# Kernel tuning notes

Hardware: AMD Instinct MI355X
Metric: run time of the kernel (lower is better)

## Reference

```python
import jax, jax.numpy as jnp
import numpy as np
import math

B, S, D, OUT, H = 512, 80, 768, 768, 12


def setup_inputs() -> dict:
    key = jax.random.key(0)
    ks = jax.random.split(key, 8)
    scale = 0.02
    hidden = jax.random.normal(ks[0], (B, S, D), dtype=jnp.float32)
    mask = jnp.ones((B, S), dtype=jnp.int32)
    Wq = jax.random.normal(ks[1], (D, D), dtype=jnp.float32) * scale
    bq = jax.random.normal(ks[2], (D,), dtype=jnp.float32) * scale
    Wk = jax.random.normal(ks[3], (D, D), dtype=jnp.float32) * scale
    bk = jax.random.normal(ks[4], (D,), dtype=jnp.float32) * scale
    Wv = jax.random.normal(ks[5], (D, OUT), dtype=jnp.float32) * scale
    bv = jax.random.normal(ks[6], (OUT,), dtype=jnp.float32) * scale
    return {"hidden": hidden, "mask": mask, "Wq": Wq, "bq": bq,
            "Wk": Wk, "bk": bk, "Wv": Wv, "bv": bv}


def _rope_tables(seq_len, head_dim, dtype):
    # RoE_QAndK(seq_len): standard RoPE, emb = cat([sin, cos], -1), chunked
    half = head_dim // 2
    inv_freq = 1.0 / (10000.0 ** (np.arange(0, half, dtype=np.float32) * 2.0 / head_dim))
    pos = np.arange(seq_len, dtype=np.float32)
    freqs = pos[:, None] * inv_freq[None, :]  # [S, half]
    return jnp.asarray(np.sin(freqs), dtype), jnp.asarray(np.cos(freqs), dtype)


def _rotate(x, sin, cos):
    # interleaved RoPE: even/odd channels
    x1, x2 = x[..., 0::2], x[..., 1::2]
    out = jnp.stack([x1 * cos - x2 * sin, x2 * cos + x1 * sin], axis=-1)
    return out.reshape(x.shape)


def reference(hidden, mask, Wq, bq, Wk, bk, Wv, bv):
    b, s, d = hidden.shape
    dh = Wq.shape[1] // H   # query/key head dim
    dv = Wv.shape[1] // H   # value head dim

    def split_heads(x, hd):
        return x.reshape(b, s, H, hd).transpose(0, 2, 1, 3)  # [b,h,s,hd]

    q = split_heads(hidden @ Wq + bq, dh)
    k = split_heads(hidden @ Wk + bk, dh)
    v = split_heads(hidden @ Wv + bv, dv)

    sin, cos = _rope_tables(s, dh, hidden.dtype)  # [s, dh//2]
    q = _rotate(q, sin, cos)
    k = _rotate(k, sin, cos)

    bias = (1.0 - mask.astype(hidden.dtype))[:, None, None, :] * -10000.0
    scores = jnp.einsum('bhqd,bhkd->bhqk', q, k) / math.sqrt(dh) + bias
    prob = jax.nn.softmax(scores, axis=-1)  # dropout is identity in eval
    ctx = jnp.einsum('bhqk,bhkd->bhqd', prob, v)
    return ctx.transpose(0, 2, 1, 3).reshape(b, s, H * dv)
```

## Files before the change

kernel.cpp:

```cpp
#include <hip/hip_runtime.h>
#include <hip/hip_bf16.h>
#include <stdint.h>

#define H_    12
#define B_    512
#define S_    80
#define D_    768
#define NQKV  2304
#define DH    64

typedef __bf16 bf16x8 __attribute__((ext_vector_type(8)));
typedef float  f32x4  __attribute__((ext_vector_type(4)));
typedef unsigned short u16;
typedef unsigned int   u32;

__device__ __forceinline__ u16 f2bf(float f) {
    u32 u = __builtin_bit_cast(u32, f);
    u32 r = u + 0x7FFFu + ((u >> 16) & 1u);
    return (u16)(r >> 16);
}
__device__ __forceinline__ float bf2f(u16 h) {
    u32 u = ((u32)h) << 16;
    return __builtin_bit_cast(float, u);
}

__device__ __forceinline__ void gload16(const void* g, void* l) {
    __builtin_amdgcn_global_load_lds((const __attribute__((address_space(1))) void*)g,
                                     (__attribute__((address_space(3))) void*)l, 16, 0, 0);
}

#define VMCNT(n) asm volatile("s_waitcnt vmcnt(" #n ")" ::: "memory")
#define BARRIER() do { asm volatile("" ::: "memory"); __builtin_amdgcn_s_barrier(); asm volatile("" ::: "memory"); } while (0)

#define TRB 432
#define CVB 1616

__global__ __launch_bounds__(256) void prep_fused(
    const float* __restrict__ X,
    const float* __restrict__ Wq, const float* __restrict__ bq,
    const float* __restrict__ Wk, const float* __restrict__ bk,
    const float* __restrict__ Wv, const float* __restrict__ bv,
    u16* __restrict__ Wt, float* __restrict__ biasf,
    float* __restrict__ ropeS, float* __restrict__ ropeC,
    u16* __restrict__ Xb)
{
    const int tid = threadIdx.x;
    if (blockIdx.x < TRB) {
        __shared__ u16 T[64][72];
        int t = blockIdx.x;
        int mat = t / 144;
        int rem = t - mat * 144;
        int kb = (rem / 12) * 64;
        int nb = (rem % 12) * 64;
        const float* W = (mat == 0) ? Wq : (mat == 1 ? Wk : Wv);
        int r  = tid >> 2;
        int q4 = tid & 3;
#pragma unroll
        for (int i = 0; i < 4; ++i) {
            float4 v = *reinterpret_cast<const float4*>(&W[(size_t)(kb + r) * D_ + nb + q4 * 16 + i * 4]);
            T[q4 * 16 + i * 4 + 0][r] = f2bf(v.x);
            T[q4 * 16 + i * 4 + 1][r] = f2bf(v.y);
            T[q4 * 16 + i * 4 + 2][r] = f2bf(v.z);
            T[q4 * 16 + i * 4 + 3][r] = f2bf(v.w);
        }
        __syncthreads();
        int n_local = tid >> 2;
        int kq = tid & 3;
        uint4 o0 = *reinterpret_cast<const uint4*>(&T[n_local][kq * 16]);
        uint4 o1 = *reinterpret_cast<const uint4*>(&T[n_local][kq * 16 + 8]);
        u16* dst = &Wt[(size_t)(mat * D_ + nb + n_local) * D_ + kb + kq * 16];
        *reinterpret_cast<uint4*>(dst) = o0;
        *reinterpret_cast<uint4*>(dst + 8) = o1;
    } else {
        int gidx = (blockIdx.x - TRB) * 256 + tid;
        const int gstride = CVB * 256;
        for (int i = gidx; i < NQKV; i += gstride) {
            const float* bsrc; int nn;
            if (i < D_)          { bsrc = bq; nn = i; }
            else if (i < 2 * D_) { bsrc = bk; nn = i - D_; }
            else                 { bsrc = bv; nn = i - 2 * D_; }
            biasf[i] = bsrc[nn];
        }
        for (int i = gidx; i < S_ * 32; i += gstride) {
            int pos = i >> 5, fi = i & 31;
            float invf = powf(10000.0f, -(float)fi / 32.0f);
            float fr = (float)pos * invf;
            ropeS[i] = sinf(fr);
            ropeC[i] = cosf(fr);
        }
        const int n4 = 40960 * D_ / 4;
        for (int i = gidx; i < n4; i += gstride) {
            float4 v = reinterpret_cast<const float4*>(X)[i];
            uint2 u;
            u.x = (u32)f2bf(v.x) | ((u32)f2bf(v.y) << 16);
            u.y = (u32)f2bf(v.z) | ((u32)f2bf(v.w) << 16);
            reinterpret_cast<uint2*>(Xb)[i] = u;
        }
    }
}

#define BK 64
#define NT 12
#define CLD 264

__global__ __launch_bounds__(512, 2) void qkv_gemm(
    const u16*   __restrict__ Xb,
    const u16*   __restrict__ Wt,
    const float* __restrict__ biasf,
    u16*         __restrict__ Y)
{
    __shared__ alignas(16) u16 smem[65536];

    const int orig = blockIdx.x;
    const int swz = (orig & 7) * 180 + (orig >> 3);
    const int m0 = (swz / 9) * 256;
    const int n0 = (swz % 9) * 256;

    const int tid = threadIdx.x;
    const int lane = tid & 63;
    const int w  = tid >> 6;
    const int wr = w >> 2;
    const int wc = w & 3;
    const int lr = lane & 15;
    const int lg = lane >> 4;

    const int srow = tid >> 3;
    const int scol = ((tid & 7) ^ (srow & 7)) << 3;

    f32x4 acc[8][4] = {};
    bf16x8 af[2][4], bf[2][4];

#define STAGE_A(p, h, q, kt) \
    gload16(&Xb[(size_t)(m0 + (h)*128 + (q)*64 + srow) * D_ + (kt)*BK + scol], \
            &smem[(p)*32768 + (h)*8192 + (q)*4096 + w*512])
#define STAGE_B(p, hb, jj, kt) \
    gload16(&Wt[(size_t)(n0 + (hb)*128 + (jj)*64 + srow) * D_ + (kt)*BK + scol], \
            &smem[(p)*32768 + 16384 + (hb)*8192 + (jj)*4096 + w*512])
#define LDA_F(p, rr, kk_) \
    (*reinterpret_cast<const bf16x8*>(&smem[(p)*32768 + wr*8192 + (rr)*64 + ((((kk_)*4 + lg) ^ ((rr) & 7)) << 3)]))
#define LDB_F(p, rb, kk_) \
    (*reinterpret_cast<const bf16x8*>(&smem[(p)*32768 + 16384 + (wc>>1)*8192 + (rb)*64 + ((((kk_)*4 + lg) ^ ((rb) & 7)) << 3)]))

    STAGE_A(0, 0, 0, 0); STAGE_A(0, 1, 0, 0);
    STAGE_B(0, 0, 0, 0); STAGE_B(0, 0, 1, 0);
    STAGE_B(0, 1, 0, 0); STAGE_B(0, 1, 1, 0);
    STAGE_A(0, 0, 1, 0); STAGE_A(0, 1, 1, 0);
    VMCNT(2);
    BARRIER();

#pragma unroll
    for (int u = 0; u < NT - 1; ++u) {
        const int p = u & 1, pn = p ^ 1, kt1 = u + 1;
#pragma unroll
        for (int kk = 0; kk < 2; ++kk) {
#pragma unroll
            for (int ii = 0; ii < 4; ++ii) af[kk][ii] = LDA_F(p, ii * 16 + lr, kk);
#pragma unroll
            for (int jj = 0; jj < 2; ++jj) bf[kk][jj] = LDB_F(p, (wc & 1) * 64 + jj * 16 + lr, kk);
        }
        STAGE_A(pn, 0, 0, kt1); STAGE_A(pn, 1, 0, kt1);
        STAGE_B(pn, 0, 0, kt1); STAGE_B(pn, 0, 1, kt1);
        BARRIER();
        __builtin_amdgcn_s_setprio(1);
#pragma unroll
        for (int kk = 0; kk < 2; ++kk)
#pragma unroll
            for (int ii = 0; ii < 4; ++ii)
#pragma unroll
                for (int jj = 0; jj < 2; ++jj)
                    acc[ii][jj] = __builtin_amdgcn_mfma_f32_16x16x32_bf16(af[kk][ii], bf[kk][jj], acc[ii][jj], 0, 0, 0);
        __builtin_amdgcn_s_setprio(0);
#pragma unroll
        for (int kk = 0; kk < 2; ++kk)
#pragma unroll
            for (int jj = 2; jj < 4; ++jj) bf[kk][jj] = LDB_F(p, (wc & 1) * 64 + jj * 16 + lr, kk);
        STAGE_B(pn, 1, 0, kt1); STAGE_B(pn, 1, 1, kt1);
        VMCNT(6);
        BARRIER();
        __builtin_amdgcn_s_setprio(1);
#pragma unroll
        for (int kk = 0; kk < 2; ++kk)
#pragma unroll
            for (int ii = 0; ii < 4; ++ii)
#pragma unroll
                for (int jj = 0; jj < 2; ++jj)
                    acc[ii][jj + 2] = __builtin_amdgcn_mfma_f32_16x16x32_bf16(af[kk][ii], bf[kk][jj + 2], acc[ii][jj + 2], 0, 0, 0);
        __builtin_amdgcn_s_setprio(0);
#pragma unroll
        for (int kk = 0; kk < 2; ++kk)
#pragma unroll
            for (int ii = 0; ii < 4; ++ii) af[kk][ii] = LDA_F(p, 64 + ii * 16 + lr, kk);
        STAGE_A(pn, 0, 1, kt1); STAGE_A(pn, 1, 1, kt1);
        BARRIER();
        __builtin_amdgcn_s_setprio(1);
#pragma unroll
        for (int kk = 0; kk < 2; ++kk)
#pragma unroll
            for (int ii = 0; ii < 4; ++ii)
#pragma unroll
                for (int jj = 0; jj < 2; ++jj)
                    acc[ii + 4][jj] = __builtin_amdgcn_mfma_f32_16x16x32_bf16(af[kk][ii], bf[kk][jj], acc[ii + 4][jj], 0, 0, 0);
        __builtin_amdgcn_s_setprio(0);
        VMCNT(2);
        BARRIER();
        __builtin_amdgcn_s_setprio(1);
#pragma unroll
        for (int kk = 0; kk < 2; ++kk)
#pragma unroll
            for (int ii = 0; ii < 4; ++ii)
#pragma unroll
                for (int jj = 0; jj < 2; ++jj)
                    acc[ii + 4][jj + 2] = __builtin_amdgcn_mfma_f32_16x16x32_bf16(af[kk][ii], bf[kk][jj + 2], acc[ii + 4][jj + 2], 0, 0, 0);
        __builtin_amdgcn_s_setprio(0);
    }
    {
        const int p = 1;
#pragma unroll
        for (int kk = 0; kk < 2; ++kk) {
#pragma unroll
            for (int ii = 0; ii < 4; ++ii) af[kk][ii] = LDA_F(p, ii * 16 + lr, kk);
#pragma unroll
            for (int jj = 0; jj < 2; ++jj) bf[kk][jj] = LDB_F(p, (wc & 1) * 64 + jj * 16 + lr, kk);
        }
        BARRIER();
#pragma unroll
        for (int kk = 0; kk < 2; ++kk)
#pragma unroll
            for (int ii = 0; ii < 4; ++ii)
#pragma unroll
                for (int jj = 0; jj < 2; ++jj)
                    acc[ii][jj] = __builtin_amdgcn_mfma_f32_16x16x32_bf16(af[kk][ii], bf[kk][jj], acc[ii][jj], 0, 0, 0);
#pragma unroll
        for (int kk = 0; kk < 2; ++kk)
#pragma unroll
            for (int jj = 2; jj < 4; ++jj) bf[kk][jj] = LDB_F(p, (wc & 1) * 64 + jj * 16 + lr, kk);
        VMCNT(0);
        BARRIER();
#pragma unroll
        for (int kk = 0; kk < 2; ++kk)
#pragma unroll
            for (int ii = 0; ii < 4; ++ii)
#pragma unroll
                for (int jj = 0; jj < 2; ++jj)
                    acc[ii][jj + 2] = __builtin_amdgcn_mfma_f32_16x16x32_bf16(af[kk][ii], bf[kk][jj + 2], acc[ii][jj + 2], 0, 0, 0);
#pragma unroll
        for (int kk = 0; kk < 2; ++kk)
#pragma unroll
            for (int ii = 0; ii < 4; ++ii) af[kk][ii] = LDA_F(p, 64 + ii * 16 + lr, kk);
        BARRIER();
#pragma unroll
        for (int kk = 0; kk < 2; ++kk)
#pragma unroll
            for (int ii = 0; ii < 4; ++ii)
#pragma unroll
                for (int jj = 0; jj < 2; ++jj)
                    acc[ii + 4][jj] = __builtin_amdgcn_mfma_f32_16x16x32_bf16(af[kk][ii], bf[kk][jj], acc[ii + 4][jj], 0, 0, 0);
        BARRIER();
#pragma unroll
        for (int kk = 0; kk < 2; ++kk)
#pragma unroll
            for (int ii = 0; ii < 4; ++ii)
#pragma unroll
                for (int jj = 0; jj < 2; ++jj)
                    acc[ii + 4][jj + 2] = __builtin_amdgcn_mfma_f32_16x16x32_bf16(af[kk][ii], bf[kk][jj + 2], acc[ii + 4][jj + 2], 0, 0, 0);
    }

    float bias_v[4];
#pragma unroll
    for (int j = 0; j < 4; ++j) bias_v[j] = biasf[n0 + wc * 64 + j * 16 + lr];

    __syncthreads();
#pragma unroll
    for (int hh = 0; hh < 2; ++hh) {
        if (wr == hh) {
#pragma unroll
            for (int i = 0; i < 8; ++i)
#pragma unroll
                for (int j = 0; j < 4; ++j)
#pragma unroll
                    for (int r = 0; r < 4; ++r)
                        smem[(i * 16 + lg * 4 + r) * CLD + wc * 64 + j * 16 + lr] = f2bf(acc[i][j][r] + bias_v[j]);
        }
        __syncthreads();
#pragma unroll
        for (int pp = 0; pp < 8; ++pp) {
            int idx = pp * 512 + tid;
            int row = idx >> 5, ch = idx & 31;
            uint4 v = *reinterpret_cast<const uint4*>(&smem[row * CLD + ch * 8]);
            *reinterpret_cast<uint4*>(&Y[(size_t)(m0 + hh * 128 + row) * NQKV + n0 + ch * 8]) = v;
        }
        __syncthreads();
    }
#undef STAGE_A
#undef STAGE_B
#undef LDA_F
#undef LDB_F
}

#define LQ 72
#define LV 104

__device__ __forceinline__ u32 rope_rot(u32 u, float sn, float cs, float scale) {
    float x1 = bf2f((u16)(u & 0xffff)), x2 = bf2f((u16)(u >> 16));
    float o1 = (x1 * cs - x2 * sn) * scale;
    float o2 = (x2 * cs + x1 * sn) * scale;
    return (u32)f2bf(o1) | ((u32)f2bf(o2) << 16);
}

__global__ __launch_bounds__(320) void attn_kernel(
    const u16* __restrict__ Y,
    const int* __restrict__ mask,
    const float* __restrict__ ropeS,
    const float* __restrict__ ropeC,
    float* __restrict__ out)
{
    __shared__ alignas(16) u16 Qs[S_ * LQ];
    __shared__ alignas(16) u16 Ks[S_ * LQ];
    __shared__ alignas(16) u16 Vt[DH * LV];
    __shared__ alignas(16) u16 Ps[5 * 16 * LV];
    __shared__ float biasS[S_];

    const int h = blockIdx.x;
    const int b = blockIdx.y;
    const int tid = threadIdx.x;
    const size_t rowbase = (size_t)b * S_ * NQKV;

#pragma unroll
    for (int it = 0; it < 4; ++it) {
        int ch = it * 320 + tid;
        int q = ch >> 4;
        int sub = ch & 15;
        int isK = sub >> 3;
        int c0 = (sub & 7) * 8;
        uint4 v = *reinterpret_cast<const uint4*>(&Y[rowbase + (size_t)q * NQKV + isK * D_ + h * DH + c0]);
        float4 sn4 = *reinterpret_cast<const float4*>(&ropeS[q * 32 + c0 / 2]);
        float4 cs4 = *reinterpret_cast<const float4*>(&ropeC[q * 32 + c0 / 2]);
        float scale = isK ? 1.0f : 0.125f;
        uint4 o;
        o.x = rope_rot(v.x, sn4.x, cs4.x, scale);
        o.y = rope_rot(v.y, sn4.y, cs4.y, scale);
        o.z = rope_rot(v.z, sn4.z, cs4.z, scale);
        o.w = rope_rot(v.w, sn4.w, cs4.w, scale);
        u16* dst = isK ? Ks : Qs;
        *reinterpret_cast<uint4*>(&dst[q * LQ + c0]) = o;
    }
#pragma unroll
    for (int it = 0; it < 2; ++it) {
        int ch = it * 320 + tid;
        int s = ch >> 3, c0 = (ch & 7) * 8;
        uint4 v = *reinterpret_cast<const uint4*>(&Y[rowbase + (size_t)s * NQKV + 2 * D_ + h * DH + c0]);
        Vt[(c0 + 0) * LV + s] = (u16)(v.x & 0xffff);
        Vt[(c0 + 1) * LV + s] = (u16)(v.x >> 16);
        Vt[(c0 + 2) * LV + s] = (u16)(v.y & 0xffff);
        Vt[(c0 + 3) * LV + s] = (u16)(v.y >> 16);
        Vt[(c0 + 4) * LV + s] = (u16)(v.z & 0xffff);
        Vt[(c0 + 5) * LV + s] = (u16)(v.z >> 16);
        Vt[(c0 + 6) * LV + s] = (u16)(v.w & 0xffff);
        Vt[(c0 + 7) * LV + s] = (u16)(v.w >> 16);
    }
    for (int e = tid; e < DH * 16; e += 320) {
        int c = e >> 4, s = 80 + (e & 15);
        Vt[c * LV + s] = 0;
    }
    for (int e = tid; e < S_ * 16; e += 320) {
        int row = e >> 4, col = 80 + (e & 15);
        Ps[row * LV + col] = 0;
    }
    for (int e = tid; e < S_; e += 320)
        biasS[e] = (1.0f - (float)mask[b * S_ + e]) * -10000.0f;
    __syncthreads();

    const int wv = tid >> 6;
    const int lane = tid & 63;
    const int lr = lane & 15;
    const int lg = lane >> 4;

    f32x4 sc[5] = {};
    bf16x8 aq[2];
#pragma unroll
    for (int kk = 0; kk < 2; ++kk)
        aq[kk] = *reinterpret_cast<const bf16x8*>(&Qs[(wv * 16 + lr) * LQ + kk * 32 + lg * 8]);
#pragma unroll
    for (int t = 0; t < 5; ++t) {
#pragma unroll
        for (int kk = 0; kk < 2; ++kk) {
            bf16x8 bk8 = *reinterpret_cast<const bf16x8*>(&Ks[(t * 16 + lr) * LQ + kk * 32 + lg * 8]);
            sc[t] = __builtin_amdgcn_mfma_f32_16x16x32_bf16(aq[kk], bk8, sc[t], 0, 0, 0);
        }
    }
#pragma unroll
    for (int j = 0; j < 4; ++j) {
        float m = -1e30f;
#pragma unroll
        for (int t = 0; t < 5; ++t) { sc[t][j] += biasS[t * 16 + lr]; m = fmaxf(m, sc[t][j]); }
#pragma unroll
        for (int msk = 1; msk < 16; msk <<= 1) m = fmaxf(m, __shfl_xor(m, msk));
        float s = 0.f;
#pragma unroll
        for (int t = 0; t < 5; ++t) { float e = __expf(sc[t][j] - m); sc[t][j] = e; s += e; }
#pragma unroll
        for (int msk = 1; msk < 16; msk <<= 1) s += __shfl_xor(s, msk);
        float ri = 1.0f / s;
#pragma unroll
        for (int t = 0; t < 5; ++t) sc[t][j] *= ri;
    }
#pragma unroll
    for (int t = 0; t < 5; ++t)
#pragma unroll
        for (int j = 0; j < 4; ++j)
            Ps[(wv * 16 + lg * 4 + j) * LV + t * 16 + lr] = f2bf(sc[t][j]);
    __syncthreads();

    f32x4 co[4] = {};
#pragma unroll
    for (int kk = 0; kk < 3; ++kk) {
        bf16x8 ap = *reinterpret_cast<const bf16x8*>(&Ps[(wv * 16 + lr) * LV + kk * 32 + lg * 8]);
#pragma unroll
        for (int t = 0; t < 4; ++t) {
            bf16x8 bv8 = *reinterpret_cast<const bf16x8*>(&Vt[(t * 16 + lr) * LV + kk * 32 + lg * 8]);
            co[t] = __builtin_amdgcn_mfma_f32_16x16x32_bf16(ap, bv8, co[t], 0, 0, 0);
        }
    }
    const size_t obase = (size_t)(b * S_ + wv * 16 + lg * 4) * D_ + h * DH;
#pragma unroll
    for (int t = 0; t < 4; ++t)
#pragma unroll
        for (int j = 0; j < 4; ++j)
            out[obase + (size_t)j * D_ + t * 16 + lr] = co[t][j];
}

extern "C" void kernel_launch(void* const* d_in, const int* in_sizes, int n_in,
                              void* d_out, int out_size, void* d_ws, size_t ws_size,
                              hipStream_t stream) {
    const float* hidden = (const float*)d_in[0];
    const int*   mask   = (const int*)d_in[1];
    const float* Wq     = (const float*)d_in[2];
    const float* bq     = (const float*)d_in[3];
    const float* Wk     = (const float*)d_in[4];
    const float* bk     = (const float*)d_in[5];
    const float* Wv     = (const float*)d_in[6];
    const float* bv     = (const float*)d_in[7];
    float* out = (float*)d_out;

    char* ws = (char*)d_ws;
    u16*   Wt    = (u16*)(ws + 0);
    float* biasf = (float*)(ws + 3538944);
    float* ropeS = (float*)(ws + 3548160);
    float* ropeC = (float*)(ws + 3558400);
    u16*   Y     = (u16*)(ws + 4194304);

    u16* Xb = (u16*)d_out;

    prep_fused<<<dim3(TRB + CVB), dim3(256), 0, stream>>>(hidden, Wq, bq, Wk, bk, Wv, bv,
                                                          Wt, biasf, ropeS, ropeC, Xb);
    qkv_gemm<<<dim3(1440), dim3(512), 0, stream>>>(Xb, Wt, biasf, Y);
    attn_kernel<<<dim3(H_, B_), dim3(320), 0, stream>>>(Y, mask, ropeS, ropeC, out);
}
```

Before: 274.0 us.

## Simplify GEMM main loop to whole-tile double buffering with one barrier

Replaces the finely interleaved 4-phase schedule (staggered partial-tile global loads, several barriers per K step, setprio hints, peeled final iteration) with a plain double-buffered loop. Each iteration now issues the full next tile's loads up front, runs all MFMAs on the current buffer, then waits for all loads and synchronises once. This cuts barrier count and code size. The cost is that load issue is no longer spread across compute phases and the MFMA priority hints are gone, so latency hiding may suffer.

```diff
diff --git a/kernel.cpp b/kernel.cpp
--- a/kernel.cpp
+++ b/kernel.cpp
@@ -140,17 +140,19 @@
     (*reinterpret_cast<const bf16x8*>(&smem[(p)*32768 + wr*8192 + (rr)*64 + ((((kk_)*4 + lg) ^ ((rr) & 7)) << 3)]))
 #define LDB_F(p, rb, kk_) \
     (*reinterpret_cast<const bf16x8*>(&smem[(p)*32768 + 16384 + (wc>>1)*8192 + (rb)*64 + ((((kk_)*4 + lg) ^ ((rb) & 7)) << 3)]))
-
-    STAGE_A(0, 0, 0, 0); STAGE_A(0, 1, 0, 0);
-    STAGE_B(0, 0, 0, 0); STAGE_B(0, 0, 1, 0);
-    STAGE_B(0, 1, 0, 0); STAGE_B(0, 1, 1, 0);
-    STAGE_A(0, 0, 1, 0); STAGE_A(0, 1, 1, 0);
-    VMCNT(2);
+#define STAGE_TILE(p, kt) do { \
+    STAGE_A(p, 0, 0, kt); STAGE_A(p, 0, 1, kt); STAGE_A(p, 1, 0, kt); STAGE_A(p, 1, 1, kt); \
+    STAGE_B(p, 0, 0, kt); STAGE_B(p, 0, 1, kt); STAGE_B(p, 1, 0, kt); STAGE_B(p, 1, 1, kt); } while (0)
+
+    STAGE_TILE(0, 0);
+    VMCNT(0);
     BARRIER();
 
 #pragma unroll
-    for (int u = 0; u < NT - 1; ++u) {
-        const int p = u & 1, pn = p ^ 1, kt1 = u + 1;
+    for (int u = 0; u < NT; ++u) {
+        const int p = u & 1;
+        if (u + 1 < NT) STAGE_TILE(p ^ 1, u + 1);
+
 #pragma unroll
         for (int kk = 0; kk < 2; ++kk) {
 #pragma unroll
@@ -158,10 +160,6 @@
 #pragma unroll
             for (int jj = 0; jj < 2; ++jj) bf[kk][jj] = LDB_F(p, (wc & 1) * 64 + jj * 16 + lr, kk);
         }
-        STAGE_A(pn, 0, 0, kt1); STAGE_A(pn, 1, 0, kt1);
-        STAGE_B(pn, 0, 0, kt1); STAGE_B(pn, 0, 1, kt1);
-        BARRIER();
-        __builtin_amdgcn_s_setprio(1);
 #pragma unroll
         for (int kk = 0; kk < 2; ++kk)
 #pragma unroll
@@ -169,15 +167,11 @@
 #pragma unroll
                 for (int jj = 0; jj < 2; ++jj)
                     acc[ii][jj] = __builtin_amdgcn_mfma_f32_16x16x32_bf16(af[kk][ii], bf[kk][jj], acc[ii][jj], 0, 0, 0);
-        __builtin_amdgcn_s_setprio(0);
+
 #pragma unroll
         for (int kk = 0; kk < 2; ++kk)
 #pragma unroll
             for (int jj = 2; jj < 4; ++jj) bf[kk][jj] = LDB_F(p, (wc & 1) * 64 + jj * 16 + lr, kk);
-        STAGE_B(pn, 1, 0, kt1); STAGE_B(pn, 1, 1, kt1);
-        VMCNT(6);
-        BARRIER();
-        __builtin_amdgcn_s_setprio(1);
 #pragma unroll
         for (int kk = 0; kk < 2; ++kk)
 #pragma unroll
@@ -185,14 +179,11 @@
 #pragma unroll
                 for (int jj = 0; jj < 2; ++jj)
                     acc[ii][jj + 2] = __builtin_amdgcn_mfma_f32_16x16x32_bf16(af[kk][ii], bf[kk][jj + 2], acc[ii][jj + 2], 0, 0, 0);
-        __builtin_amdgcn_s_setprio(0);
+
 #pragma unroll
         for (int kk = 0; kk < 2; ++kk)
 #pragma unroll
             for (int ii = 0; ii < 4; ++ii) af[kk][ii] = LDA_F(p, 64 + ii * 16 + lr, kk);
-        STAGE_A(pn, 0, 1, kt1); STAGE_A(pn, 1, 1, kt1);
-        BARRIER();
-        __builtin_amdgcn_s_setprio(1);
 #pragma unroll
         for (int kk = 0; kk < 2; ++kk)
 #pragma unroll
@@ -200,10 +191,6 @@
 #pragma unroll
                 for (int jj = 0; jj < 2; ++jj)
                     acc[ii + 4][jj] = __builtin_amdgcn_mfma_f32_16x16x32_bf16(af[kk][ii], bf[kk][jj], acc[ii + 4][jj], 0, 0, 0);
-        __builtin_amdgcn_s_setprio(0);
-        VMCNT(2);
-        BARRIER();
-        __builtin_amdgcn_s_setprio(1);
 #pragma unroll
         for (int kk = 0; kk < 2; ++kk)
 #pragma unroll
@@ -211,65 +198,15 @@
 #pragma unroll
                 for (int jj = 0; jj < 2; ++jj)
                     acc[ii + 4][jj + 2] = __builtin_amdgcn_mfma_f32_16x16x32_bf16(af[kk][ii], bf[kk][jj + 2], acc[ii + 4][jj + 2], 0, 0, 0);
-        __builtin_amdgcn_s_setprio(0);
-    }
-    {
-        const int p = 1;
-#pragma unroll
-        for (int kk = 0; kk < 2; ++kk) {
-#pragma unroll
-            for (int ii = 0; ii < 4; ++ii) af[kk][ii] = LDA_F(p, ii * 16 + lr, kk);
-#pragma unroll
-            for (int jj = 0; jj < 2; ++jj) bf[kk][jj] = LDB_F(p, (wc & 1) * 64 + jj * 16 + lr, kk);
-        }
-        BARRIER();
-#pragma unroll
-        for (int kk = 0; kk < 2; ++kk)
-#pragma unroll
-            for (int ii = 0; ii < 4; ++ii)
-#pragma unroll
-                for (int jj = 0; jj < 2; ++jj)
-                    acc[ii][jj] = __builtin_amdgcn_mfma_f32_16x16x32_bf16(af[kk][ii], bf[kk][jj], acc[ii][jj], 0, 0, 0);
-#pragma unroll
-        for (int kk = 0; kk < 2; ++kk)
-#pragma unroll
-            for (int jj = 2; jj < 4; ++jj) bf[kk][jj] = LDB_F(p, (wc & 1) * 64 + jj * 16 + lr, kk);
+
         VMCNT(0);
         BARRIER();
-#pragma unroll
-        for (int kk = 0; kk < 2; ++kk)
-#pragma unroll
-            for (int ii = 0; ii < 4; ++ii)
-#pragma unroll
-                for (int jj = 0; jj < 2; ++jj)
-                    acc[ii][jj + 2] = __builtin_amdgcn_mfma_f32_16x16x32_bf16(af[kk][ii], bf[kk][jj + 2], acc[ii][jj + 2], 0, 0, 0);
-#pragma unroll
-        for (int kk = 0; kk < 2; ++kk)
-#pragma unroll
-            for (int ii = 0; ii < 4; ++ii) af[kk][ii] = LDA_F(p, 64 + ii * 16 + lr, kk);
-        BARRIER();
-#pragma unroll
-        for (int kk = 0; kk < 2; ++kk)
-#pragma unroll
-            for (int ii = 0; ii < 4; ++ii)
-#pragma unroll
-                for (int jj = 0; jj < 2; ++jj)
-                    acc[ii + 4][jj] = __builtin_amdgcn_mfma_f32_16x16x32_bf16(af[kk][ii], bf[kk][jj], acc[ii + 4][jj], 0, 0, 0);
-        BARRIER();
-#pragma unroll
-        for (int kk = 0; kk < 2; ++kk)
-#pragma unroll
-            for (int ii = 0; ii < 4; ++ii)
-#pragma unroll
-                for (int jj = 0; jj < 2; ++jj)
-                    acc[ii + 4][jj + 2] = __builtin_amdgcn_mfma_f32_16x16x32_bf16(af[kk][ii], bf[kk][jj + 2], acc[ii + 4][jj + 2], 0, 0, 0);
     }
 
     float bias_v[4];
 #pragma unroll
     for (int j = 0; j < 4; ++j) bias_v[j] = biasf[n0 + wc * 64 + j * 16 + lr];
 
-    __syncthreads();
 #pragma unroll
     for (int hh = 0; hh < 2; ++hh) {
         if (wr == hh) {
@@ -293,6 +230,7 @@
     }
 #undef STAGE_A
 #undef STAGE_B
+#undef STAGE_TILE
 #undef LDA_F
 #undef LDB_F
 }
```

Result: no change. 277.6 us (+1.3%).
